# Performance work log

Measured on AMD Instinct MI355X. Metric: run time of the kernel, lower is better.

## Reference

```python
import math
import jax, jax.numpy as jnp
import numpy as np

S, D, E = 8192, 2048, 64            # tokens, model_dim, num_experts
CAPACITY_FACTOR = 1.0
CAP = int(CAPACITY_FACTOR * math.ceil(S / E))  # 128, static (training-mode 'drop' gate)


def setup_inputs() -> dict:
    key = jax.random.key(0)
    kx, kw = jax.random.split(key)
    x = jax.random.normal(kx, (S, D), dtype=jnp.float32)
    wg = jax.random.normal(kw, (E, D), dtype=jnp.float32) * 0.02  # Linear(D, E, bias=False) weight
    return {"x": x, "wg": wg}


def reference(x, wg):
    # logits = self.wg(input)
    logits = jnp.einsum('sd,ed->se', x, wg)                 # [S, E]
    gates = jax.nn.softmax(logits, axis=1)                  # [S, E]
    indices1_s = jnp.argmax(gates, axis=1)                  # [S]
    mask1 = jax.nn.one_hot(indices1_s, E, dtype=gates.dtype)  # [S, E]

    # load-balancing aux loss
    me = jnp.mean(gates, axis=0)
    ce = jnp.mean(mask1, axis=0)
    l_aux = jnp.mean(me * ce) * (E * E)

    # gates1_s computed BEFORE capacity drop (as in source)
    gates1_s = jnp.sum(gates * mask1, axis=1)               # [S]

    # fused_cumsum_sub_one: position of each token within its expert's queue
    locations1 = jnp.cumsum(mask1, axis=0) - 1.0            # [S, E]
    # capacity drop ('drop' gate type)
    mask1 = mask1 * (locations1 < CAP).astype(mask1.dtype)
    locations1_s = jnp.sum(locations1 * mask1, axis=1).astype(jnp.int32)  # [S]

    gates1 = gates1_s[:, None] * mask1                      # [S, E]
    locations1_sc = jax.nn.one_hot(locations1_s, CAP, dtype=gates1.dtype)  # [S, CAP]
    # bmm(gates1[:,:,None], loc_sc[:,None,:]) == outer product per token
    combine1_sec = jnp.einsum('se,sc->sec', gates1, locations1_sc)  # [S, E, CAP]
    dispatch_mask = combine1_sec.astype(bool)
    return l_aux, combine1_sec, dispatch_mask
```

## Files before the change

### kernel.cpp

```cpp
#include <hip/hip_runtime.h>
#include <cstddef>
#include <cstdint>

#define S_TOK 8192
#define DDIM  2048
#define NEXP  64
#define CAPTY 128
#define KC    64
#define TPB   64
#define NBLK  (S_TOK / TPB)
#define SPLITK 8
#define KPER  (DDIM / SPLITK)
#define SEC   ((size_t)S_TOK * NEXP * CAPTY)

__global__ __launch_bounds__(256)
void gate_gemm_kernel(const float* __restrict__ x, const float* __restrict__ wg,
                      float* __restrict__ part)
{
    __shared__ float xs[TPB][72];
    __shared__ float ws[KC][NEXP];

    const int tid = threadIdx.x;
    const int el  = tid & 15;
    const int tg  = tid >> 4;
    const int kp  = blockIdx.x & (SPLITK - 1);
    const int tc  = blockIdx.x >> 3;
    const int t_base = tc * TPB;
    const int k_base = kp * KPER;

    float acc[4][4];
#pragma unroll
    for (int i = 0; i < 4; ++i)
#pragma unroll
        for (int j = 0; j < 4; ++j) acc[i][j] = 0.0f;

    for (int kc0 = 0; kc0 < KPER; kc0 += KC) {
        const int kc = k_base + kc0;
        __syncthreads();
#pragma unroll
        for (int m = 0; m < 4; ++m) {
            int idx = tid + 256 * m;
            int t = idx >> 4;
            int c = idx & 15;
            float4 v = *(const float4*)(x + (size_t)(t_base + t) * DDIM + kc + c * 4);
            *(float4*)&xs[t][c * 4] = v;
        }
#pragma unroll
        for (int m = 0; m < 4; ++m) {
            int idx = tid + 256 * m;
            int e = idx & 63;
            int c = idx >> 6;
            float4 w = *(const float4*)(wg + (size_t)e * DDIM + kc + c * 4);
            ws[c * 4 + 0][e] = w.x;
            ws[c * 4 + 1][e] = w.y;
            ws[c * 4 + 2][e] = w.z;
            ws[c * 4 + 3][e] = w.w;
        }
        __syncthreads();

#pragma unroll
        for (int k4 = 0; k4 < KC; k4 += 4) {
            float4 xv[4], wv[4];
#pragma unroll
            for (int i = 0; i < 4; ++i)
                xv[i] = *(const float4*)&xs[tg + 16 * i][k4];
#pragma unroll
            for (int j = 0; j < 4; ++j)
                wv[j] = *(const float4*)&ws[k4 + j][el * 4];
#pragma unroll
            for (int i = 0; i < 4; ++i) {
                acc[i][0] += xv[i].x * wv[0].x; acc[i][1] += xv[i].x * wv[0].y;
                acc[i][2] += xv[i].x * wv[0].z; acc[i][3] += xv[i].x * wv[0].w;
                acc[i][0] += xv[i].y * wv[1].x; acc[i][1] += xv[i].y * wv[1].y;
                acc[i][2] += xv[i].y * wv[1].z; acc[i][3] += xv[i].y * wv[1].w;
                acc[i][0] += xv[i].z * wv[2].x; acc[i][1] += xv[i].z * wv[2].y;
                acc[i][2] += xv[i].z * wv[2].z; acc[i][3] += xv[i].z * wv[2].w;
                acc[i][0] += xv[i].w * wv[3].x; acc[i][1] += xv[i].w * wv[3].y;
                acc[i][2] += xv[i].w * wv[3].z; acc[i][3] += xv[i].w * wv[3].w;
            }
        }
    }

#pragma unroll
    for (int i = 0; i < 4; ++i) {
        int t = tg + 16 * i;
        float4 v = make_float4(acc[i][0], acc[i][1], acc[i][2], acc[i][3]);
        *(float4*)(part + ((size_t)kp * S_TOK + t_base + t) * NEXP + el * 4) = v;
    }
}

__global__ __launch_bounds__(256)
void softmax_kernel(const float* __restrict__ part,
                    float* __restrict__ gate_s, int* __restrict__ expert,
                    int* __restrict__ rank, int* __restrict__ hist,
                    float* __restrict__ partial_g)
{
    __shared__ float probs[TPB][NEXP + 1];
    __shared__ int   sexp[TPB];

    const int tid = threadIdx.x;
    const int t_base = blockIdx.x * TPB;
    const int t = tid >> 2, q = tid & 3;
    const int tok = t_base + t;

#pragma unroll
    for (int jj = 0; jj < 4; ++jj) {
        float4 a = make_float4(0.f, 0.f, 0.f, 0.f);
#pragma unroll
        for (int kpp = 0; kpp < SPLITK; ++kpp) {
            float4 v = *(const float4*)(part + ((size_t)kpp * S_TOK + tok) * NEXP + q * 16 + jj * 4);
            a.x += v.x; a.y += v.y; a.z += v.z; a.w += v.w;
        }
        probs[t][q * 16 + jj * 4 + 0] = a.x;
        probs[t][q * 16 + jj * 4 + 1] = a.y;
        probs[t][q * 16 + jj * 4 + 2] = a.z;
        probs[t][q * 16 + jj * 4 + 3] = a.w;
    }
    __syncthreads();

    if (tid < TPB) {
        const int t2 = tid, tok2 = t_base + t2;
        float m = -1e30f; int am = 0;
        for (int e = 0; e < NEXP; ++e) {
            float v = probs[t2][e];
            if (v > m) { m = v; am = e; }
        }
        float s = 0.0f;
        for (int e = 0; e < NEXP; ++e) s += __expf(probs[t2][e] - m);
        float rcp = 1.0f / s;
        for (int e = 0; e < NEXP; ++e)
            probs[t2][e] = __expf(probs[t2][e] - m) * rcp;
        sexp[t2] = am;
        gate_s[tok2] = rcp;
        expert[tok2] = am;
    }
    __syncthreads();

    if (tid < TPB) {
        const int t2 = tid;
        const int am = sexp[t2];
        int r = 0;
        for (int u = 0; u < t2; ++u) r += (sexp[u] == am) ? 1 : 0;
        rank[t_base + t2] = r;
    } else if (tid < 2 * TPB) {
        const int e = tid - TPB;
        float pg = 0.0f; int cnt = 0;
        for (int u = 0; u < TPB; ++u) {
            pg  += probs[u][e];
            cnt += (sexp[u] == e) ? 1 : 0;
        }
        partial_g[blockIdx.x * NEXP + e] = pg;
        hist[blockIdx.x * NEXP + e]      = cnt;
    }
}

__global__ __launch_bounds__(64)
void scan_kernel(const int* __restrict__ hist, const float* __restrict__ partial_g,
                 int* __restrict__ chunk_base, float* __restrict__ l_aux_ws)
{
    int e = threadIdx.x;
    int base = 0;
    float sg = 0.0f;
    for (int c = 0; c < NBLK; ++c) {
        chunk_base[c * NEXP + e] = base;
        base += hist[c * NEXP + e];
        sg   += partial_g[c * NEXP + e];
    }
    float v = sg * (float)base;
#pragma unroll
    for (int off = 32; off > 0; off >>= 1) v += __shfl_down(v, off);
    if (e == 0)
        l_aux_ws[0] = v * (64.0f / (8192.0f * 8192.0f));
}

__global__ __launch_bounds__(256)
void scatter_kernel(const float* __restrict__ gate_s, const int* __restrict__ expert,
                    const int* __restrict__ rank, const int* __restrict__ chunk_base,
                    const float* __restrict__ l_aux_ws, float* __restrict__ out)
{
    int s = blockIdx.x * 256 + threadIdx.x;
    if (s == 0) out[0] = l_aux_ws[0];
    if (s >= S_TOK) return;
    int e   = expert[s];
    int loc = chunk_base[(s >> 6) * NEXP + e] + rank[s];
    if (loc < CAPTY) {
        size_t idx = 1 + (size_t)s * (NEXP * CAPTY) + (size_t)e * CAPTY + loc;
        out[idx]       = gate_s[s];
        out[idx + SEC] = 1.0f;
    }
}

extern "C" void kernel_launch(void* const* d_in, const int* in_sizes, int n_in,
                              void* d_out, int out_size, void* d_ws, size_t ws_size,
                              hipStream_t stream)
{
    const float* x  = (const float*)d_in[0];
    const float* wg = (const float*)d_in[1];
    float* out = (float*)d_out;
    char* ws = (char*)d_ws;

    float* part      = (float*)(ws + 0);
    size_t off = (size_t)SPLITK * S_TOK * NEXP * sizeof(float);
    float* gate_s    = (float*)(ws + off);          off += 32768;
    int*   expert    = (int*)  (ws + off);          off += 32768;
    int*   rank      = (int*)  (ws + off);          off += 32768;
    int*   hist      = (int*)  (ws + off);          off += 32768;
    float* partial_g = (float*)(ws + off);          off += 32768;
    int*   chunk_b   = (int*)  (ws + off);          off += 32768;
    float* l_aux_ws  = (float*)(ws + off);

    gate_gemm_kernel<<<NBLK * SPLITK, 256, 0, stream>>>(x, wg, part);
    softmax_kernel<<<NBLK, 256, 0, stream>>>(part, gate_s, expert, rank, hist, partial_g);
    scan_kernel<<<1, 64, 0, stream>>>(hist, partial_g, chunk_b, l_aux_ws);
    hipMemsetAsync(d_out, 0, (size_t)out_size * sizeof(float), stream);
    scatter_kernel<<<(S_TOK + 255) / 256, 256, 0, stream>>>(gate_s, expert, rank,
                                                            chunk_b, l_aux_ws, out);
}
```

Baseline: 595.5 us.

## Fuse gate GEMM, softmax and output zero-fill into one kernel

Replaces the split-K gate GEMM, the separate softmax kernel and the hipMemset with a single kernel. 128 blocks compute the full-K logits and the softmax/rank/histogram directly from registers through a shared-memory union, so the split-K partial buffer is never written or read back. The remaining 896 blocks zero-fill the large output at the same time, and the GEMM blocks zero the tail once they finish. This trades the parallelism of split-K (only 128 GEMM blocks now) for overlapping the memory-bound zero-fill with the compute and for fewer launches.

Result: slower. 762.8 us (+28.1%).

```diff
diff --git a/kernel.cpp b/kernel.cpp
--- a/kernel.cpp
+++ b/kernel.cpp
@@ -8,25 +8,41 @@
 #define CAPTY 128
 #define KC    64
 #define TPB   64
-#define NBLK  (S_TOK / TPB)
-#define SPLITK 8
-#define KPER  (DDIM / SPLITK)
+#define NBLK  128
+#define NFILL 896
+#define NTOT  1024
 #define SEC   ((size_t)S_TOK * NEXP * CAPTY)
+#define FILL4_PER_FILLBLK 36864
+#define FILL4_PER_GEMMBLK 4096
+#define FILL4_GEMM_BASE   ((size_t)NFILL * FILL4_PER_FILLBLK)
+
+struct GemmSm { float xs[TPB][72]; float ws2[KC][NEXP]; };
+struct SoftSm { float probs[TPB][NEXP + 1]; int sexp[TPB]; };
+union SMemU { GemmSm g; SoftSm s; };
 
 __global__ __launch_bounds__(256)
-void gate_gemm_kernel(const float* __restrict__ x, const float* __restrict__ wg,
-                      float* __restrict__ part)
-{
-    __shared__ float xs[TPB][72];
-    __shared__ float ws[KC][NEXP];
-
+void mega_kernel(const float* __restrict__ x, const float* __restrict__ wg,
+                 float* __restrict__ gate_s, int* __restrict__ expert,
+                 int* __restrict__ rank, int* __restrict__ hist,
+                 float* __restrict__ partial_g, float* __restrict__ out)
+{
+    __shared__ SMemU sm;
     const int tid = threadIdx.x;
-    const int el  = tid & 15;
-    const int tg  = tid >> 4;
-    const int kp  = blockIdx.x & (SPLITK - 1);
-    const int tc  = blockIdx.x >> 3;
-    const int t_base = tc * TPB;
-    const int k_base = kp * KPER;
+    const int bid = blockIdx.x;
+    float4* out4 = (float4*)out;
+    const float4 z = make_float4(0.f, 0.f, 0.f, 0.f);
+
+    if (bid >= NBLK) {
+        const size_t base = (size_t)(bid - NBLK) * FILL4_PER_FILLBLK;
+#pragma unroll 4
+        for (int it = 0; it < FILL4_PER_FILLBLK / 256; ++it)
+            out4[base + (size_t)it * 256 + tid] = z;
+        return;
+    }
+
+    const int el = tid & 15;
+    const int tg = tid >> 4;
+    const int t_base = bid * TPB;
 
     float acc[4][4];
 #pragma unroll
@@ -34,8 +50,7 @@
 #pragma unroll
         for (int j = 0; j < 4; ++j) acc[i][j] = 0.0f;
 
-    for (int kc0 = 0; kc0 < KPER; kc0 += KC) {
-        const int kc = k_base + kc0;
+    for (int kc = 0; kc < DDIM; kc += KC) {
         __syncthreads();
 #pragma unroll
         for (int m = 0; m < 4; ++m) {
@@ -43,7 +58,7 @@
             int t = idx >> 4;
             int c = idx & 15;
             float4 v = *(const float4*)(x + (size_t)(t_base + t) * DDIM + kc + c * 4);
-            *(float4*)&xs[t][c * 4] = v;
+            *(float4*)&sm.g.xs[t][c * 4] = v;
         }
 #pragma unroll
         for (int m = 0; m < 4; ++m) {
@@ -51,10 +66,10 @@
             int e = idx & 63;
             int c = idx >> 6;
             float4 w = *(const float4*)(wg + (size_t)e * DDIM + kc + c * 4);
-            ws[c * 4 + 0][e] = w.x;
-            ws[c * 4 + 1][e] = w.y;
-            ws[c * 4 + 2][e] = w.z;
-            ws[c * 4 + 3][e] = w.w;
+            sm.g.ws2[c * 4 + 0][e] = w.x;
+            sm.g.ws2[c * 4 + 1][e] = w.y;
+            sm.g.ws2[c * 4 + 2][e] = w.z;
+            sm.g.ws2[c * 4 + 3][e] = w.w;
         }
         __syncthreads();
 
@@ -63,10 +78,10 @@
             float4 xv[4], wv[4];
 #pragma unroll
             for (int i = 0; i < 4; ++i)
-                xv[i] = *(const float4*)&xs[tg + 16 * i][k4];
+                xv[i] = *(const float4*)&sm.g.xs[tg + 16 * i][k4];
 #pragma unroll
             for (int j = 0; j < 4; ++j)
-                wv[j] = *(const float4*)&ws[k4 + j][el * 4];
+                wv[j] = *(const float4*)&sm.g.ws2[k4 + j][el * 4];
 #pragma unroll
             for (int i = 0; i < 4; ++i) {
                 acc[i][0] += xv[i].x * wv[0].x; acc[i][1] += xv[i].x * wv[0].y;
@@ -81,56 +96,27 @@
         }
     }
 
-#pragma unroll
-    for (int i = 0; i < 4; ++i) {
-        int t = tg + 16 * i;
-        float4 v = make_float4(acc[i][0], acc[i][1], acc[i][2], acc[i][3]);
-        *(float4*)(part + ((size_t)kp * S_TOK + t_base + t) * NEXP + el * 4) = v;
-    }
-}
-
-__global__ __launch_bounds__(256)
-void softmax_kernel(const float* __restrict__ part,
-                    float* __restrict__ gate_s, int* __restrict__ expert,
-                    int* __restrict__ rank, int* __restrict__ hist,
-                    float* __restrict__ partial_g)
-{
-    __shared__ float probs[TPB][NEXP + 1];
-    __shared__ int   sexp[TPB];
-
-    const int tid = threadIdx.x;
-    const int t_base = blockIdx.x * TPB;
-    const int t = tid >> 2, q = tid & 3;
-    const int tok = t_base + t;
-
-#pragma unroll
-    for (int jj = 0; jj < 4; ++jj) {
-        float4 a = make_float4(0.f, 0.f, 0.f, 0.f);
-#pragma unroll
-        for (int kpp = 0; kpp < SPLITK; ++kpp) {
-            float4 v = *(const float4*)(part + ((size_t)kpp * S_TOK + tok) * NEXP + q * 16 + jj * 4);
-            a.x += v.x; a.y += v.y; a.z += v.z; a.w += v.w;
-        }
-        probs[t][q * 16 + jj * 4 + 0] = a.x;
-        probs[t][q * 16 + jj * 4 + 1] = a.y;
-        probs[t][q * 16 + jj * 4 + 2] = a.z;
-        probs[t][q * 16 + jj * 4 + 3] = a.w;
-    }
+    __syncthreads();
+#pragma unroll
+    for (int i = 0; i < 4; ++i)
+#pragma unroll
+        for (int j = 0; j < 4; ++j)
+            sm.s.probs[tg + 16 * i][el * 4 + j] = acc[i][j];
     __syncthreads();
 
     if (tid < TPB) {
         const int t2 = tid, tok2 = t_base + t2;
         float m = -1e30f; int am = 0;
         for (int e = 0; e < NEXP; ++e) {
-            float v = probs[t2][e];
+            float v = sm.s.probs[t2][e];
             if (v > m) { m = v; am = e; }
         }
         float s = 0.0f;
-        for (int e = 0; e < NEXP; ++e) s += __expf(probs[t2][e] - m);
+        for (int e = 0; e < NEXP; ++e) s += __expf(sm.s.probs[t2][e] - m);
         float rcp = 1.0f / s;
         for (int e = 0; e < NEXP; ++e)
-            probs[t2][e] = __expf(probs[t2][e] - m) * rcp;
-        sexp[t2] = am;
+            sm.s.probs[t2][e] = __expf(sm.s.probs[t2][e] - m) * rcp;
+        sm.s.sexp[t2] = am;
         gate_s[tok2] = rcp;
         expert[tok2] = am;
     }
@@ -138,19 +124,27 @@
 
     if (tid < TPB) {
         const int t2 = tid;
-        const int am = sexp[t2];
+        const int am = sm.s.sexp[t2];
         int r = 0;
-        for (int u = 0; u < t2; ++u) r += (sexp[u] == am) ? 1 : 0;
+        for (int u = 0; u < t2; ++u) r += (sm.s.sexp[u] == am) ? 1 : 0;
         rank[t_base + t2] = r;
     } else if (tid < 2 * TPB) {
         const int e = tid - TPB;
         float pg = 0.0f; int cnt = 0;
         for (int u = 0; u < TPB; ++u) {
-            pg  += probs[u][e];
-            cnt += (sexp[u] == e) ? 1 : 0;
-        }
-        partial_g[blockIdx.x * NEXP + e] = pg;
-        hist[blockIdx.x * NEXP + e]      = cnt;
+            pg  += sm.s.probs[u][e];
+            cnt += (sm.s.sexp[u] == e) ? 1 : 0;
+        }
+        partial_g[bid * NEXP + e] = pg;
+        hist[bid * NEXP + e]      = cnt;
+    }
+
+    {
+        const size_t base = FILL4_GEMM_BASE + (size_t)bid * FILL4_PER_GEMMBLK;
+#pragma unroll 4
+        for (int it = 0; it < FILL4_PER_GEMMBLK / 256; ++it)
+            out4[base + (size_t)it * 256 + tid] = z;
+        if (bid == 0 && tid == 0) out[2 * SEC] = 0.0f;
     }
 }
 
@@ -199,8 +193,7 @@
     float* out = (float*)d_out;
     char* ws = (char*)d_ws;
 
-    float* part      = (float*)(ws + 0);
-    size_t off = (size_t)SPLITK * S_TOK * NEXP * sizeof(float);
+    size_t off = 0;
     float* gate_s    = (float*)(ws + off);          off += 32768;
     int*   expert    = (int*)  (ws + off);          off += 32768;
     int*   rank      = (int*)  (ws + off);          off += 32768;
@@ -209,10 +202,9 @@
     int*   chunk_b   = (int*)  (ws + off);          off += 32768;
     float* l_aux_ws  = (float*)(ws + off);
 
-    gate_gemm_kernel<<<NBLK * SPLITK, 256, 0, stream>>>(x, wg, part);
-    softmax_kernel<<<NBLK, 256, 0, stream>>>(part, gate_s, expert, rank, hist, partial_g);
+    mega_kernel<<<NTOT, 256, 0, stream>>>(x, wg, gate_s, expert, rank,
+                                          hist, partial_g, out);
     scan_kernel<<<1, 64, 0, stream>>>(hist, partial_g, chunk_b, l_aux_ws);
-    hipMemsetAsync(d_out, 0, (size_t)out_size * sizeof(float), stream);
     scatter_kernel<<<(S_TOK + 255) / 256, 256, 0, stream>>>(gate_s, expert, rank,
                                                             chunk_b, l_aux_ws, out);
 }
```

## Prefetch next GEMM tile into registers and fuse scan with scatter kernel

Applied to the files above, without the earlier changes.

The gate GEMM now loads the next K chunk of x and wg into registers while the current chunk is computed from shared memory, so global load latency overlaps the math. The separate single-block scan kernel and the scatter kernel are merged into one single-block kernel that keeps chunk bases in shared memory and writes l_aux directly. This removes a kernel launch and a round trip through global memory. The cost is that the scatter now runs on only 256 threads in one block, and the GEMM uses more registers.

Result: slower. 646.0 us (+8.5%).

```diff
diff --git a/kernel.cpp b/kernel.cpp
--- a/kernel.cpp
+++ b/kernel.cpp
@@ -28,6 +28,18 @@
     const int t_base = tc * TPB;
     const int k_base = kp * KPER;
 
+    const float* xbase = x + (size_t)t_base * DDIM + k_base;
+    const float* wbase = wg + k_base;
+    const int we  = tid & 63;
+    const int wc0 = tid >> 6;
+
+    float4 xr[4], wr[4];
+#pragma unroll
+    for (int m = 0; m < 4; ++m) {
+        xr[m] = *(const float4*)(xbase + (size_t)(tg + 16 * m) * DDIM + el * 4);
+        wr[m] = *(const float4*)(wbase + (size_t)we * DDIM + (wc0 + 4 * m) * 4);
+    }
+
     float acc[4][4];
 #pragma unroll
     for (int i = 0; i < 4; ++i)
@@ -35,26 +47,22 @@
         for (int j = 0; j < 4; ++j) acc[i][j] = 0.0f;
 
     for (int kc0 = 0; kc0 < KPER; kc0 += KC) {
-        const int kc = k_base + kc0;
         __syncthreads();
 #pragma unroll
         for (int m = 0; m < 4; ++m) {
-            int idx = tid + 256 * m;
-            int t = idx >> 4;
-            int c = idx & 15;
-            float4 v = *(const float4*)(x + (size_t)(t_base + t) * DDIM + kc + c * 4);
-            *(float4*)&xs[t][c * 4] = v;
-        }
-#pragma unroll
-        for (int m = 0; m < 4; ++m) {
-            int idx = tid + 256 * m;
-            int e = idx & 63;
-            int c = idx >> 6;
-            float4 w = *(const float4*)(wg + (size_t)e * DDIM + kc + c * 4);
-            ws[c * 4 + 0][e] = w.x;
-            ws[c * 4 + 1][e] = w.y;
-            ws[c * 4 + 2][e] = w.z;
-            ws[c * 4 + 3][e] = w.w;
+            *(float4*)&xs[tg + 16 * m][el * 4] = xr[m];
+            const int c = wc0 + 4 * m;
+            ws[c * 4 + 0][we] = wr[m].x;
+            ws[c * 4 + 1][we] = wr[m].y;
+            ws[c * 4 + 2][we] = wr[m].z;
+            ws[c * 4 + 3][we] = wr[m].w;
+        }
+        if (kc0 + KC < KPER) {
+#pragma unroll
+            for (int m = 0; m < 4; ++m) {
+                xr[m] = *(const float4*)(xbase + (size_t)(tg + 16 * m) * DDIM + kc0 + KC + el * 4);
+                wr[m] = *(const float4*)(wbase + (size_t)we * DDIM + kc0 + KC + (wc0 + 4 * m) * 4);
+            }
         }
         __syncthreads();
 
@@ -154,39 +162,38 @@
     }
 }
 
-__global__ __launch_bounds__(64)
-void scan_kernel(const int* __restrict__ hist, const float* __restrict__ partial_g,
-                 int* __restrict__ chunk_base, float* __restrict__ l_aux_ws)
-{
-    int e = threadIdx.x;
-    int base = 0;
-    float sg = 0.0f;
-    for (int c = 0; c < NBLK; ++c) {
-        chunk_base[c * NEXP + e] = base;
-        base += hist[c * NEXP + e];
-        sg   += partial_g[c * NEXP + e];
-    }
-    float v = sg * (float)base;
-#pragma unroll
-    for (int off = 32; off > 0; off >>= 1) v += __shfl_down(v, off);
-    if (e == 0)
-        l_aux_ws[0] = v * (64.0f / (8192.0f * 8192.0f));
-}
-
 __global__ __launch_bounds__(256)
-void scatter_kernel(const float* __restrict__ gate_s, const int* __restrict__ expert,
-                    const int* __restrict__ rank, const int* __restrict__ chunk_base,
-                    const float* __restrict__ l_aux_ws, float* __restrict__ out)
-{
-    int s = blockIdx.x * 256 + threadIdx.x;
-    if (s == 0) out[0] = l_aux_ws[0];
-    if (s >= S_TOK) return;
-    int e   = expert[s];
-    int loc = chunk_base[(s >> 6) * NEXP + e] + rank[s];
-    if (loc < CAPTY) {
-        size_t idx = 1 + (size_t)s * (NEXP * CAPTY) + (size_t)e * CAPTY + loc;
-        out[idx]       = gate_s[s];
-        out[idx + SEC] = 1.0f;
+void scan_scatter_kernel(const int* __restrict__ hist, const float* __restrict__ partial_g,
+                         const float* __restrict__ gate_s, const int* __restrict__ expert,
+                         const int* __restrict__ rank, float* __restrict__ out)
+{
+    __shared__ int base_s[NBLK][NEXP];
+    const int tid = threadIdx.x;
+
+    if (tid < NEXP) {
+        const int e = tid;
+        int base = 0; float sg = 0.0f;
+#pragma unroll 16
+        for (int c = 0; c < NBLK; ++c) {
+            base_s[c][e] = base;
+            base += hist[c * NEXP + e];
+            sg  += partial_g[c * NEXP + e];
+        }
+        float v = sg * (float)base;
+#pragma unroll
+        for (int off = 32; off > 0; off >>= 1) v += __shfl_down(v, off);
+        if (e == 0) out[0] = v * (64.0f / (8192.0f * 8192.0f));
+    }
+    __syncthreads();
+
+    for (int s = tid; s < S_TOK; s += 256) {
+        const int e = expert[s];
+        const int loc = base_s[s >> 6][e] + rank[s];
+        if (loc < CAPTY) {
+            size_t idx = 1 + (size_t)s * (NEXP * CAPTY) + (size_t)e * CAPTY + loc;
+            out[idx]       = gate_s[s];
+            out[idx + SEC] = 1.0f;
+        }
     }
 }
 
@@ -205,14 +212,10 @@
     int*   expert    = (int*)  (ws + off);          off += 32768;
     int*   rank      = (int*)  (ws + off);          off += 32768;
     int*   hist      = (int*)  (ws + off);          off += 32768;
-    float* partial_g = (float*)(ws + off);          off += 32768;
-    int*   chunk_b   = (int*)  (ws + off);          off += 32768;
-    float* l_aux_ws  = (float*)(ws + off);
+    float* partial_g = (float*)(ws + off);
 
     gate_gemm_kernel<<<NBLK * SPLITK, 256, 0, stream>>>(x, wg, part);
     softmax_kernel<<<NBLK, 256, 0, stream>>>(part, gate_s, expert, rank, hist, partial_g);
-    scan_kernel<<<1, 64, 0, stream>>>(hist, partial_g, chunk_b, l_aux_ws);
     hipMemsetAsync(d_out, 0, (size_t)out_size * sizeof(float), stream);
-    scatter_kernel<<<(S_TOK + 255) / 256, 256, 0, stream>>>(gate_s, expert, rank,
-                                                            chunk_b, l_aux_ws, out);
-}
+    scan_scatter_kernel<<<1, 256, 0, stream>>>(hist, partial_g, gate_s, expert, rank, out);
+}
```
